# Kernel optimization log

Hardware: AMD Instinct MI355X
Metric: run time of the kernel (lower is better)

## Reference

```python
import jax, jax.numpy as jnp
import numpy as np
import math

B, T, C, H = 2, 2048, 1024, 16
HD = C // H  # head dim = 64

def setup_inputs() -> dict:
    key = jax.random.key(0)
    ks = jax.random.split(key, 12)
    s = 0.02
    return {
        "x": jax.random.normal(ks[0], (B, T, C), dtype=jnp.float32),
        "ln1_g": jnp.ones((C,), jnp.float32),
        "ln1_b": jnp.zeros((C,), jnp.float32),
        "W_attn": jax.random.normal(ks[1], (C, 3 * C), jnp.float32) * s,
        "b_attn": jnp.zeros((3 * C,), jnp.float32),
        "W_ap": jax.random.normal(ks[2], (C, C), jnp.float32) * s,
        "b_ap": jnp.zeros((C,), jnp.float32),
        "ln2_g": jnp.ones((C,), jnp.float32),
        "ln2_b": jnp.zeros((C,), jnp.float32),
        "W_fc": jax.random.normal(ks[3], (C, 4 * C), jnp.float32) * s,
        "b_fc": jnp.zeros((4 * C,), jnp.float32),
        "W_mp": jax.random.normal(ks[4], (4 * C, C), jnp.float32) * s,
        "b_mp": jnp.zeros((C,), jnp.float32),
    }

def layernorm(x, g, b, eps=1e-5):
    mu = jnp.mean(x, axis=-1, keepdims=True)
    var = jnp.mean(jnp.square(x - mu), axis=-1, keepdims=True)
    return (x - mu) * jax.lax.rsqrt(var + eps) * g + b

def gelu_tanh(x):
    # GELU(approximate='tanh')
    c = math.sqrt(2.0 / math.pi)
    return 0.5 * x * (1.0 + jnp.tanh(c * (x + 0.044715 * x * x * x)))

def attention(x, W_attn, b_attn, W_ap, b_ap):
    b, t, c = x.shape
    qkv = x @ W_attn + b_attn                      # [B,T,3C]
    q, k, v = jnp.split(qkv, 3, axis=-1)
    q = q.reshape(b, t, H, HD).transpose(0, 2, 1, 3)  # [B,H,T,hd]
    k = k.reshape(b, t, H, HD).transpose(0, 2, 1, 3)
    v = v.reshape(b, t, H, HD).transpose(0, 2, 1, 3)
    attn = jnp.einsum('bhqd,bhkd->bhqk', q, k) * (1.0 / math.sqrt(HD))
    mask = jnp.tril(jnp.ones((t, t), dtype=bool))
    attn = jnp.where(mask, attn, jnp.float32(-jnp.inf))
    attn = jax.nn.softmax(attn, axis=-1)
    y = jnp.einsum('bhqk,bhkd->bhqd', attn, v)
    y = y.transpose(0, 2, 1, 3).reshape(b, t, c)
    return y @ W_ap + b_ap

def reference(x, ln1_g, ln1_b, W_attn, b_attn, W_ap, b_ap,
              ln2_g, ln2_b, W_fc, b_fc, W_mp, b_mp):
    x = x + attention(layernorm(x, ln1_g, ln1_b), W_attn, b_attn, W_ap, b_ap)
    h = layernorm(x, ln2_g, ln2_b)
    h = gelu_tanh(h @ W_fc + b_fc) @ W_mp + b_mp
    return x + h
```

## Files before the change

kernel.cpp:

```cpp
#include <hip/hip_runtime.h>
#include <stdint.h>

#define TT_ 2048
#define CC_ 1024

typedef unsigned short u16;
typedef __bf16 bf16x8 __attribute__((ext_vector_type(8)));
typedef __bf16 bf16x4 __attribute__((ext_vector_type(4)));
typedef float f32x4 __attribute__((ext_vector_type(4)));
typedef unsigned short u16x8 __attribute__((ext_vector_type(8)));

__device__ __forceinline__ u16 f2bf(float f) {
  unsigned u = __float_as_uint(f);
  u += 0x7fff + ((u >> 16) & 1);
  return (u16)(u >> 16);
}
__device__ __forceinline__ float bf2f(u16 v) {
  return __uint_as_float(((unsigned)v) << 16);
}

__device__ __forceinline__ float gelu_f(float t) {
  float u = 1.5957691216057308f * (t + 0.044715f * t * t * t);
  return t / (1.f + __expf(-u));
}

__device__ __forceinline__ void async_cp16(const u16* g, u16* l) {
  __builtin_amdgcn_global_load_lds(
      (const __attribute__((address_space(1))) void*)(uintptr_t)g,
      (__attribute__((address_space(3))) void*)(uint32_t)(uintptr_t)l,
      16, 0, 0);
}

__device__ __forceinline__ void blockbar() {
  asm volatile("" ::: "memory");
  __builtin_amdgcn_s_barrier();
  asm volatile("" ::: "memory");
}

__global__ __launch_bounds__(256) void kconv_t(const float* __restrict__ W,
                                               u16* __restrict__ WT, int K, int N) {
  __shared__ float t[32][33];
  int n0 = blockIdx.x * 32, k0 = blockIdx.y * 32;
  int tx = threadIdx.x & 31, ty = threadIdx.x >> 5;
#pragma unroll
  for (int r = 0; r < 4; ++r)
    t[ty + 8 * r][tx] = W[(size_t)(k0 + ty + 8 * r) * N + n0 + tx];
  __syncthreads();
#pragma unroll
  for (int r = 0; r < 4; ++r)
    WT[(size_t)(n0 + ty + 8 * r) * K + k0 + tx] = f2bf(t[tx][ty + 8 * r]);
}

__global__ __launch_bounds__(256) void kln(const float* __restrict__ x,
                                           const float* __restrict__ g,
                                           const float* __restrict__ b,
                                           u16* __restrict__ out) {
  int row = blockIdx.x, tid = threadIdx.x;
  const float4* xr = (const float4*)(x + (size_t)row * CC_);
  float4 v = xr[tid];
  float s = v.x + v.y + v.z + v.w;
  float s2 = v.x * v.x + v.y * v.y + v.z * v.z + v.w * v.w;
#pragma unroll
  for (int off = 32; off; off >>= 1) { s += __shfl_down(s, off); s2 += __shfl_down(s2, off); }
  __shared__ float rs[4], rq[4];
  int w = tid >> 6;
  if ((tid & 63) == 0) { rs[w] = s; rq[w] = s2; }
  __syncthreads();
  s = rs[0] + rs[1] + rs[2] + rs[3];
  s2 = rq[0] + rq[1] + rq[2] + rq[3];
  float mean = s * (1.f / CC_);
  float var = s2 * (1.f / CC_) - mean * mean;
  float rstd = rsqrtf(var + 1e-5f);
  float4 gv = ((const float4*)g)[tid];
  float4 bv = ((const float4*)b)[tid];
  u16* orow = out + (size_t)row * CC_ + tid * 4;
  orow[0] = f2bf((v.x - mean) * rstd * gv.x + bv.x);
  orow[1] = f2bf((v.y - mean) * rstd * gv.y + bv.y);
  orow[2] = f2bf((v.z - mean) * rstd * gv.z + bv.z);
  orow[3] = f2bf((v.w - mean) * rstd * gv.w + bv.w);
}

template <int EPI, int NSPLIT>
__global__ __launch_bounds__(256) void kgemm(const u16* __restrict__ A,
                                             const u16* __restrict__ BTm,
                                             const float* __restrict__ bias,
                                             const float* __restrict__ resid,
                                             void* __restrict__ out,
                                             float* __restrict__ part,
                                             int M, int N, int Ktot) {
  __shared__ __align__(16) u16 As[2][128 * 32];
  __shared__ __align__(16) u16 Bs[2][128 * 32];
  const int tid = threadIdx.x, lane = tid & 63, w = tid >> 6;
  const int llo = lane & 15, lhi = lane >> 4;
  const int row0 = blockIdx.y * 128, col0 = blockIdx.x * 128;
  const int wr = w >> 1, wc = w & 1;
  const int crow = lane >> 2;
  const int ck = (lane & 3) * 8;
  const int Kc = Ktot / NSPLIT;
  const int klo = (NSPLIT > 1) ? blockIdx.z * Kc : 0;

  f32x4 acc[4][4] = {};

  auto stage = [&](int bufi, int kof) {
#pragma unroll
    for (int c = w; c < 8; c += 4) {
      int r = c * 16 + crow;
      async_cp16(A + (size_t)(row0 + r) * Ktot + klo + kof + ck, &As[bufi][c * 512]);
      async_cp16(BTm + (size_t)(col0 + r) * Ktot + klo + kof + ck, &Bs[bufi][c * 512]);
    }
  };

  const int nt = Kc / 32;
  stage(0, 0);
  asm volatile("s_waitcnt vmcnt(0)" ::: "memory");
  blockbar();
  int cur = 0;

  for (int t = 0; t < nt; ++t) {
    if (t + 1 < nt) stage(cur ^ 1, (t + 1) * 32);
    bf16x8 af[4], bfr[4];
#pragma unroll
    for (int m = 0; m < 4; ++m)
      af[m] = *(const bf16x8*)&As[cur][(wr * 64 + m * 16 + llo) * 32 + lhi * 8];
#pragma unroll
    for (int n = 0; n < 4; ++n)
      bfr[n] = *(const bf16x8*)&Bs[cur][(wc * 64 + n * 16 + llo) * 32 + lhi * 8];
#pragma unroll
    for (int m = 0; m < 4; ++m)
#pragma unroll
      for (int n = 0; n < 4; ++n)
        acc[m][n] = __builtin_amdgcn_mfma_f32_16x16x32_bf16(af[m], bfr[n], acc[m][n], 0, 0, 0);
    if (t + 1 < nt) {
      asm volatile("s_waitcnt vmcnt(0)" ::: "memory");
      blockbar();
    }
    cur ^= 1;
  }

  const int c_row = row0 + wr * 64 + lhi * 4;
  const int c_col = col0 + wc * 64 + llo;
  const bool fin = (NSPLIT == 1) || (blockIdx.z == 0);
#pragma unroll
  for (int n = 0; n < 4; ++n) {
    int col = c_col + n * 16;
    float bb = bias[col];
#pragma unroll
    for (int m = 0; m < 4; ++m) {
      f32x4 a = acc[m][n];
#pragma unroll
      for (int i = 0; i < 4; ++i) {
        size_t idx = (size_t)(c_row + m * 16 + i) * N + col;
        if (!fin) {
          part[idx] = a[i];
        } else {
          float val = a[i] + bb;
          if constexpr (EPI == 1) {
            ((float*)out)[idx] = val + resid[idx];
          } else if constexpr (EPI == 2) {
            ((u16*)out)[idx] = f2bf(gelu_f(val));
          } else {
            ((u16*)out)[idx] = f2bf(val);
          }
        }
      }
    }
  }
}

template <int EPI, int NSPLIT>
__global__ __launch_bounds__(512, 2) void kgemm2(const u16* __restrict__ A,
                                                 const u16* __restrict__ BTm,
                                                 const float* __restrict__ bias,
                                                 const float* __restrict__ resid,
                                                 void* __restrict__ out,
                                                 u16* __restrict__ part,
                                                 int M, int N, int Ktot) {
  __shared__ __align__(16) u16 LB[4][2][8192];
  const int tid = threadIdx.x, lane = tid & 63, w = tid >> 6;
  const int llo = lane & 15, lhi = lane >> 4;
  const int wr = w >> 2, wc = w & 3;
  const int row0 = blockIdx.y * 256, col0 = blockIdx.x * 256;
  const int Kc = Ktot / NSPLIT;
  const int klo = (NSPLIT > 1) ? blockIdx.z * Kc : 0;
  const int nt = Kc / 32;

  const int wsA = w & 3;
  const int hbB = (wc >> 1);
  const int wsB = (w & 1) + ((w >> 2) << 1);

  const u16 *gA[2], *gB[2];
  int ldsA[2], ldsB[2];
#pragma unroll
  for (int l = 0; l < 2; ++l) {
    int c = l * 256 + wsA * 64 + lane;
    int rowl = c >> 2;
    int kc = ((c & 3) ^ ((c >> 3) & 3)) * 8;
    gA[l] = A + (size_t)(row0 + wr * 128 + rowl) * Ktot + klo + kc;
    ldsA[l] = wr * 4096 + (l * 256 + wsA * 64) * 8;
    int c2 = l * 256 + wsB * 64 + lane;
    int row2 = c2 >> 2;
    int kc2 = ((c2 & 3) ^ ((c2 >> 3) & 3)) * 8;
    gB[l] = BTm + (size_t)(col0 + hbB * 128 + row2) * Ktot + klo + kc2;
    ldsB[l] = hbB * 4096 + (l * 256 + wsB * 64) * 8;
  }

  auto stage = [&](int t) {
    int slot = t & 3;
#pragma unroll
    for (int l = 0; l < 2; ++l) {
      async_cp16(gA[l] + (size_t)t * 32, &LB[slot][0][ldsA[l]]);
      async_cp16(gB[l] + (size_t)t * 32, &LB[slot][1][ldsB[l]]);
    }
  };

  f32x4 acc[8][4] = {};
  for (int t = 0; t < 3 && t < nt; ++t) stage(t);
  const int swz = (llo >> 1) & 3;
  const int aoffb = wr * 4096 + llo * 32 + (lhi ^ swz) * 8;
  const int boffb = hbB * 4096 + ((wc & 1) * 64 + llo) * 32 + (lhi ^ swz) * 8;

  for (int t = 0; t < nt; ++t) {
    const int slot = t & 3;
    const int rem = nt - 1 - t;
    if (rem >= 2)      asm volatile("s_waitcnt vmcnt(8)" ::: "memory");
    else if (rem == 1) asm volatile("s_waitcnt vmcnt(4)" ::: "memory");
    else               asm volatile("s_waitcnt vmcnt(0)" ::: "memory");
    asm volatile("s_waitcnt lgkmcnt(0)" ::: "memory");
    blockbar();
    if (t + 3 < nt) stage(t + 3);

    bf16x8 af[8], bfv[4];
#pragma unroll
    for (int n = 0; n < 4; ++n)
      bfv[n] = *(const bf16x8*)&LB[slot][1][boffb + n * 512];
#pragma unroll
    for (int m = 0; m < 8; ++m)
      af[m] = *(const bf16x8*)&LB[slot][0][aoffb + m * 512];
    __builtin_amdgcn_s_setprio(1);
#pragma unroll
    for (int m = 0; m < 8; ++m)
#pragma unroll
      for (int n = 0; n < 4; ++n)
        acc[m][n] = __builtin_amdgcn_mfma_f32_16x16x32_bf16(af[m], bfv[n], acc[m][n], 0, 0, 0);
    __builtin_amdgcn_s_setprio(0);
  }

  const int c_row0 = row0 + wr * 128 + lhi * 4;
  const int c_col0 = col0 + wc * 64 + llo;
  const bool fin = (NSPLIT == 1) || (blockIdx.z == 0);
  u16* pb = part + (NSPLIT > 1 ? ((size_t)(blockIdx.z - 1)) * M * N : 0);
#pragma unroll
  for (int n = 0; n < 4; ++n) {
    int col = c_col0 + n * 16;
    float bb = bias[col];
#pragma unroll
    for (int m = 0; m < 8; ++m) {
      f32x4 a = acc[m][n];
#pragma unroll
      for (int i = 0; i < 4; ++i) {
        size_t idx = (size_t)(c_row0 + m * 16 + i) * N + col;
        if (!fin) {
          pb[idx] = f2bf(a[i]);
        } else {
          float val = a[i] + bb;
          if constexpr (EPI == 1) {
            ((float*)out)[idx] = val + resid[idx];
          } else if constexpr (EPI == 2) {
            ((u16*)out)[idx] = f2bf(gelu_f(val));
          } else {
            ((u16*)out)[idx] = f2bf(val);
          }
        }
      }
    }
  }
}

__global__ __launch_bounds__(256) void kadd3(float* __restrict__ out,
                                             const u16* __restrict__ p, size_t MN) {
  size_t i0 = ((size_t)blockIdx.x * 256 + threadIdx.x) * 8;
  float4 o0 = *(float4*)(out + i0);
  float4 o1 = *(float4*)(out + i0 + 4);
#pragma unroll
  for (int s = 0; s < 3; ++s) {
    u16x8 v = *(const u16x8*)(p + s * MN + i0);
    o0.x += bf2f(v[0]); o0.y += bf2f(v[1]); o0.z += bf2f(v[2]); o0.w += bf2f(v[3]);
    o1.x += bf2f(v[4]); o1.y += bf2f(v[5]); o1.z += bf2f(v[6]); o1.w += bf2f(v[7]);
  }
  *(float4*)(out + i0) = o0;
  *(float4*)(out + i0 + 4) = o1;
}

__global__ __launch_bounds__(256) void kvtrans(const u16* __restrict__ qkv,
                                               u16* __restrict__ VT) {
  int tt = blockIdx.x;
  int bh = blockIdx.y;
  int b = bh >> 4, h = bh & 15;
  __shared__ u16 t[64][72];
  int r = threadIdx.x >> 3, c0 = (threadIdx.x & 7) * 8;
  const u16* src = qkv + (size_t)(b * TT_ + tt * 64) * 3072 + 2048 + h * 64;
#pragma unroll
  for (int it = 0; it < 2; ++it) {
    int rr = r + it * 32;
    *(u16x8*)&t[rr][c0] = *(const u16x8*)(src + (size_t)rr * 3072 + c0);
  }
  __syncthreads();
  u16* dst = VT + ((size_t)bh * 64) * TT_ + tt * 64;
#pragma unroll
  for (int it = 0; it < 2; ++it) {
    int d = r + it * 32;
    u16x8 v;
#pragma unroll
    for (int e = 0; e < 8; ++e) v[e] = t[c0 + e][d];
    *(u16x8*)(dst + (size_t)d * TT_ + c0) = v;
  }
}

__global__ __launch_bounds__(256, 4) void kattn(const u16* __restrict__ qkv,
                                                const u16* __restrict__ VT,
                                                u16* __restrict__ y) {
  const int h = blockIdx.x, b = blockIdx.y, z = blockIdx.z;
  const int tid = threadIdx.x, lane = tid & 63, w = tid >> 6;
  const int llo = lane & 15, lhi = lane >> 4;

  __shared__ __align__(16) u16 Qs[64 * 64];
  __shared__ __align__(16) u16 Ks[2][64 * 64];
  __shared__ __align__(16) u16 Vs[2][64 * 64];
  __shared__ __align__(16) u16 Ps[64 * 72];

  const size_t tok0 = (size_t)b * TT_;
  const u16* qb = qkv + tok0 * 3072 + h * 64;
  const u16* kb = qb + 1024;

  const u16 *kg[2], *vg[2];
#pragma unroll
  for (int it = 0; it < 2; ++it) {
    int p_ = w * 16 + it * 8 + (lane >> 3);
    int krow = ((p_ & 15) << 2) | (p_ >> 4);
    int scol = ((lane & 7) * 8) ^ ((p_ & 7) << 3);
    kg[it] = kb + (size_t)krow * 3072 + scol;
    vg[it] = VT + ((size_t)(b * 16 + h) * 64 + p_) * TT_ + scol;
  }

  auto stageKV = [&](int bufi, int j) {
    async_cp16(kg[0] + (size_t)j * (64 * 3072), &Ks[bufi][(w * 16 + 0) * 64]);
    async_cp16(kg[1] + (size_t)j * (64 * 3072), &Ks[bufi][(w * 16 + 8) * 64]);
    async_cp16(vg[0] + (size_t)j * 64, &Vs[bufi][(w * 16 + 0) * 64]);
    async_cp16(vg[1] + (size_t)j * 64, &Vs[bufi][(w * 16 + 8) * 64]);
  };

  const float alpha = 0.18033688011112042f;
  const int r8 = tid >> 3, ce = (tid & 7) * 8;

#pragma unroll 1
  for (int ph = 0; ph < 2; ++ph) {
    const int qt = ph ? (31 - z) : z;
    const int q0 = qt * 64;

#pragma unroll
    for (int it = 0; it < 2; ++it) {
      int tk = it * 32 + r8;
      u16x8 v = *(const u16x8*)(qb + (size_t)(q0 + tk) * 3072 + ce);
#pragma unroll
      for (int e = 0; e < 8; ++e) v[e] = f2bf(bf2f(v[e]) * alpha);
      *(u16x8*)&Qs[tk * 64 + (ce ^ ((tk & 7) << 3))] = v;
    }
    asm volatile("s_waitcnt lgkmcnt(0)" ::: "memory");
    stageKV(0, 0);
    blockbar();

    bf16x8 aq[2];
#pragma unroll
    for (int kk = 0; kk < 2; ++kk)
      aq[kk] = *(const bf16x8*)&Qs[(w * 16 + llo) * 64 +
                                   ((kk * 32 + lhi * 8) ^ ((llo & 7) << 3))];

    float m_i[4], l_i[4];
    f32x4 o[4] = {};
#pragma unroll
    for (int i = 0; i < 4; ++i) { m_i[i] = -1e30f; l_i[i] = 0.f; }

    int buf = 0;
    for (int j = 0; j <= qt; ++j) {
      if (j < qt) {
        stageKV(buf ^ 1, j + 1);
        asm volatile("s_waitcnt vmcnt(4)" ::: "memory");
      } else {
        asm volatile("s_waitcnt vmcnt(0)" ::: "memory");
      }
      blockbar();

      f32x4 s[4] = {};
      __builtin_amdgcn_s_setprio(1);
#pragma unroll
      for (int nb = 0; nb < 4; ++nb)
#pragma unroll
        for (int kk = 0; kk < 2; ++kk) {
          bf16x8 bk = *(const bf16x8*)&Ks[buf][(nb * 16 + llo) * 64 +
                                              ((kk * 32 + lhi * 8) ^ ((llo & 7) << 3))];
          s[nb] = __builtin_amdgcn_mfma_f32_16x16x32_bf16(aq[kk], bk, s[nb], 0, 0, 0);
        }
      __builtin_amdgcn_s_setprio(0);

      float sc[4][4];
      if (j == qt) {
#pragma unroll
        for (int nb = 0; nb < 4; ++nb)
#pragma unroll
          for (int i = 0; i < 4; ++i) {
            float v = s[nb][i];
            if (llo * 4 + nb > w * 16 + lhi * 4 + i) v = -1e30f;
            sc[nb][i] = v;
          }
      } else {
#pragma unroll
        for (int nb = 0; nb < 4; ++nb)
#pragma unroll
          for (int i = 0; i < 4; ++i) sc[nb][i] = s[nb][i];
      }

      float rm[4];
#pragma unroll
      for (int i = 0; i < 4; ++i) {
        float r = fmaxf(fmaxf(sc[0][i], sc[1][i]), fmaxf(sc[2][i], sc[3][i]));
#pragma unroll
        for (int off = 1; off < 16; off <<= 1) r = fmaxf(r, __shfl_xor(r, off));
        rm[i] = r;
      }

      bool need = (rm[0] > m_i[0] + 8.f) | (rm[1] > m_i[1] + 8.f) |
                  (rm[2] > m_i[2] + 8.f) | (rm[3] > m_i[3] + 8.f);
      if (__any(need)) {
#pragma unroll
        for (int i = 0; i < 4; ++i) {
          float mn = fmaxf(m_i[i], rm[i]);
          float corr = exp2f(m_i[i] - mn);
          l_i[i] *= corr;
#pragma unroll
          for (int db = 0; db < 4; ++db) o[db][i] *= corr;
          m_i[i] = mn;
        }
      }

#pragma unroll
      for (int i = 0; i < 4; ++i) {
        float p0 = exp2f(sc[0][i] - m_i[i]);
        float p1 = exp2f(sc[1][i] - m_i[i]);
        float p2 = exp2f(sc[2][i] - m_i[i]);
        float p3 = exp2f(sc[3][i] - m_i[i]);
        l_i[i] += (p0 + p1) + (p2 + p3);
        bf16x4 pk = {(__bf16)p0, (__bf16)p1, (__bf16)p2, (__bf16)p3};
        *(bf16x4*)&Ps[(w * 16 + lhi * 4 + i) * 72 + llo * 4] = pk;
      }

      bf16x8 pa[2];
#pragma unroll
      for (int kk = 0; kk < 2; ++kk)
        pa[kk] = *(const bf16x8*)&Ps[(w * 16 + llo) * 72 + kk * 32 + lhi * 8];
      __builtin_amdgcn_s_setprio(1);
#pragma unroll
      for (int db = 0; db < 4; ++db)
#pragma unroll
        for (int kk = 0; kk < 2; ++kk) {
          bf16x8 bv = *(const bf16x8*)&Vs[buf][(db * 16 + llo) * 64 +
                                              ((kk * 32 + lhi * 8) ^ ((llo & 7) << 3))];
          o[db] = __builtin_amdgcn_mfma_f32_16x16x32_bf16(pa[kk], bv, o[db], 0, 0, 0);
        }
      __builtin_amdgcn_s_setprio(0);
      blockbar();
      buf ^= 1;
    }

#pragma unroll
    for (int i = 0; i < 4; ++i) {
      float t = l_i[i];
#pragma unroll
      for (int off = 1; off < 16; off <<= 1) t += __shfl_xor(t, off);
      float inv = 1.f / t;
      size_t row = tok0 + q0 + w * 16 + lhi * 4 + i;
#pragma unroll
      for (int db = 0; db < 4; ++db)
        y[row * CC_ + h * 64 + db * 16 + llo] = f2bf(o[db][i] * inv);
    }
  }
}

extern "C" void kernel_launch(void* const* d_in, const int* in_sizes, int n_in,
                              void* d_out, int out_size, void* d_ws, size_t ws_size,
                              hipStream_t stream) {
  (void)in_sizes; (void)n_in; (void)out_size; (void)ws_size;
  const float* x      = (const float*)d_in[0];
  const float* ln1g   = (const float*)d_in[1];
  const float* ln1b   = (const float*)d_in[2];
  const float* W_attn = (const float*)d_in[3];
  const float* b_attn = (const float*)d_in[4];
  const float* W_ap   = (const float*)d_in[5];
  const float* b_ap   = (const float*)d_in[6];
  const float* ln2g   = (const float*)d_in[7];
  const float* ln2b   = (const float*)d_in[8];
  const float* W_fc   = (const float*)d_in[9];
  const float* b_fc   = (const float*)d_in[10];
  const float* W_mp   = (const float*)d_in[11];
  const float* b_mp   = (const float*)d_in[12];

  char* p = (char*)d_ws;
  u16* WTmp   = (u16*)p; p += (size_t)4096 * 1024 * 2;
  u16* WTattn = (u16*)p; p += (size_t)3072 * 1024 * 2;
  u16* WTap   = (u16*)p; p += (size_t)1024 * 1024 * 2;
  u16* WTfc   = (u16*)p; p += (size_t)4096 * 1024 * 2;
  u16* xn     = (u16*)p; p += (size_t)4096 * 1024 * 2;
  u16* qkvb   = (u16*)p; p += (size_t)4096 * 3072 * 2;
  u16* yb     = (u16*)p; p += (size_t)4096 * 1024 * 2;
  float* x1   = (float*)p; p += (size_t)4096 * 1024 * 4;
  u16* h2     = (u16*)p; p += (size_t)4096 * 1024 * 2;
  u16* fcb    = qkvb;
  u16* VT     = (u16*)x1;
  u16* mpp    = WTattn;

  kconv_t<<<dim3(96, 32), 256, 0, stream>>>(W_attn, WTattn, 1024, 3072);
  kconv_t<<<dim3(32, 32), 256, 0, stream>>>(W_ap, WTap, 1024, 1024);
  kconv_t<<<dim3(128, 32), 256, 0, stream>>>(W_fc, WTfc, 1024, 4096);
  kconv_t<<<dim3(32, 128), 256, 0, stream>>>(W_mp, WTmp, 4096, 1024);

  kln<<<4096, 256, 0, stream>>>(x, ln1g, ln1b, xn);
  kgemm<0, 1><<<dim3(24, 32), 256, 0, stream>>>(xn, WTattn, b_attn, nullptr, qkvb, nullptr, 4096, 3072, 1024);
  kvtrans<<<dim3(32, 32), 256, 0, stream>>>(qkvb, VT);
  kattn<<<dim3(16, 2, 16), 256, 0, stream>>>(qkvb, VT, yb);
  kgemm<1, 1><<<dim3(8, 32), 256, 0, stream>>>(yb, WTap, b_ap, x, x1, nullptr, 4096, 1024, 1024);
  kln<<<4096, 256, 0, stream>>>(x1, ln2g, ln2b, h2);
  kgemm2<2, 1><<<dim3(16, 16), 512, 0, stream>>>(h2, WTfc, b_fc, nullptr, fcb, nullptr, 4096, 4096, 1024);
  kgemm2<1, 4><<<dim3(4, 16, 4), 512, 0, stream>>>(fcb, WTmp, b_mp, x1, (float*)d_out, mpp, 4096, 1024, 4096);
  kadd3<<<2048, 256, 0, stream>>>((float*)d_out, mpp, (size_t)4096 * 1024);
}
```

Measured before the change: 273.8 us.

## Replace 256-tile GEMM with 128-tile kernel and split-K the attention projection

Deletes the 256x256 four-stage pipelined kgemm2 kernel and runs the FC and MLP-projection GEMMs on the simpler 128x128 double-buffered kgemm. The attention output projection is now split-K by two, with bf16 partials reduced by a generalized add kernel. kgemm's partial buffer changes from fp32 to bf16 per-split slabs. This gives more blocks for occupancy but loses the larger tile's data reuse and deeper pipeline, and adds an extra reduction pass plus bf16 rounding of the partial sums.

```diff
diff --git a/kernel.cpp b/kernel.cpp
--- a/kernel.cpp
+++ b/kernel.cpp
@@ -86,7 +86,7 @@
                                              const float* __restrict__ bias,
                                              const float* __restrict__ resid,
                                              void* __restrict__ out,
-                                             float* __restrict__ part,
+                                             u16* __restrict__ part,
                                              int M, int N, int Ktot) {
   __shared__ __align__(16) u16 As[2][128 * 32];
   __shared__ __align__(16) u16 Bs[2][128 * 32];
@@ -140,6 +140,7 @@
   const int c_row = row0 + wr * 64 + lhi * 4;
   const int c_col = col0 + wc * 64 + llo;
   const bool fin = (NSPLIT == 1) || (blockIdx.z == 0);
+  u16* pb = part + (NSPLIT > 1 ? ((size_t)(blockIdx.z > 0 ? blockIdx.z - 1 : 0)) * M * N : 0);
 #pragma unroll
   for (int n = 0; n < 4; ++n) {
     int col = c_col + n * 16;
@@ -150,115 +151,6 @@
 #pragma unroll
       for (int i = 0; i < 4; ++i) {
         size_t idx = (size_t)(c_row + m * 16 + i) * N + col;
-        if (!fin) {
-          part[idx] = a[i];
-        } else {
-          float val = a[i] + bb;
-          if constexpr (EPI == 1) {
-            ((float*)out)[idx] = val + resid[idx];
-          } else if constexpr (EPI == 2) {
-            ((u16*)out)[idx] = f2bf(gelu_f(val));
-          } else {
-            ((u16*)out)[idx] = f2bf(val);
-          }
-        }
-      }
-    }
-  }
-}
-
-template <int EPI, int NSPLIT>
-__global__ __launch_bounds__(512, 2) void kgemm2(const u16* __restrict__ A,
-                                                 const u16* __restrict__ BTm,
-                                                 const float* __restrict__ bias,
-                                                 const float* __restrict__ resid,
-                                                 void* __restrict__ out,
-                                                 u16* __restrict__ part,
-                                                 int M, int N, int Ktot) {
-  __shared__ __align__(16) u16 LB[4][2][8192];
-  const int tid = threadIdx.x, lane = tid & 63, w = tid >> 6;
-  const int llo = lane & 15, lhi = lane >> 4;
-  const int wr = w >> 2, wc = w & 3;
-  const int row0 = blockIdx.y * 256, col0 = blockIdx.x * 256;
-  const int Kc = Ktot / NSPLIT;
-  const int klo = (NSPLIT > 1) ? blockIdx.z * Kc : 0;
-  const int nt = Kc / 32;
-
-  const int wsA = w & 3;
-  const int hbB = (wc >> 1);
-  const int wsB = (w & 1) + ((w >> 2) << 1);
-
-  const u16 *gA[2], *gB[2];
-  int ldsA[2], ldsB[2];
-#pragma unroll
-  for (int l = 0; l < 2; ++l) {
-    int c = l * 256 + wsA * 64 + lane;
-    int rowl = c >> 2;
-    int kc = ((c & 3) ^ ((c >> 3) & 3)) * 8;
-    gA[l] = A + (size_t)(row0 + wr * 128 + rowl) * Ktot + klo + kc;
-    ldsA[l] = wr * 4096 + (l * 256 + wsA * 64) * 8;
-    int c2 = l * 256 + wsB * 64 + lane;
-    int row2 = c2 >> 2;
-    int kc2 = ((c2 & 3) ^ ((c2 >> 3) & 3)) * 8;
-    gB[l] = BTm + (size_t)(col0 + hbB * 128 + row2) * Ktot + klo + kc2;
-    ldsB[l] = hbB * 4096 + (l * 256 + wsB * 64) * 8;
-  }
-
-  auto stage = [&](int t) {
-    int slot = t & 3;
-#pragma unroll
-    for (int l = 0; l < 2; ++l) {
-      async_cp16(gA[l] + (size_t)t * 32, &LB[slot][0][ldsA[l]]);
-      async_cp16(gB[l] + (size_t)t * 32, &LB[slot][1][ldsB[l]]);
-    }
-  };
-
-  f32x4 acc[8][4] = {};
-  for (int t = 0; t < 3 && t < nt; ++t) stage(t);
-  const int swz = (llo >> 1) & 3;
-  const int aoffb = wr * 4096 + llo * 32 + (lhi ^ swz) * 8;
-  const int boffb = hbB * 4096 + ((wc & 1) * 64 + llo) * 32 + (lhi ^ swz) * 8;
-
-  for (int t = 0; t < nt; ++t) {
-    const int slot = t & 3;
-    const int rem = nt - 1 - t;
-    if (rem >= 2)      asm volatile("s_waitcnt vmcnt(8)" ::: "memory");
-    else if (rem == 1) asm volatile("s_waitcnt vmcnt(4)" ::: "memory");
-    else               asm volatile("s_waitcnt vmcnt(0)" ::: "memory");
-    asm volatile("s_waitcnt lgkmcnt(0)" ::: "memory");
-    blockbar();
-    if (t + 3 < nt) stage(t + 3);
-
-    bf16x8 af[8], bfv[4];
-#pragma unroll
-    for (int n = 0; n < 4; ++n)
-      bfv[n] = *(const bf16x8*)&LB[slot][1][boffb + n * 512];
-#pragma unroll
-    for (int m = 0; m < 8; ++m)
-      af[m] = *(const bf16x8*)&LB[slot][0][aoffb + m * 512];
-    __builtin_amdgcn_s_setprio(1);
-#pragma unroll
-    for (int m = 0; m < 8; ++m)
-#pragma unroll
-      for (int n = 0; n < 4; ++n)
-        acc[m][n] = __builtin_amdgcn_mfma_f32_16x16x32_bf16(af[m], bfv[n], acc[m][n], 0, 0, 0);
-    __builtin_amdgcn_s_setprio(0);
-  }
-
-  const int c_row0 = row0 + wr * 128 + lhi * 4;
-  const int c_col0 = col0 + wc * 64 + llo;
-  const bool fin = (NSPLIT == 1) || (blockIdx.z == 0);
-  u16* pb = part + (NSPLIT > 1 ? ((size_t)(blockIdx.z - 1)) * M * N : 0);
-#pragma unroll
-  for (int n = 0; n < 4; ++n) {
-    int col = c_col0 + n * 16;
-    float bb = bias[col];
-#pragma unroll
-    for (int m = 0; m < 8; ++m) {
-      f32x4 a = acc[m][n];
-#pragma unroll
-      for (int i = 0; i < 4; ++i) {
-        size_t idx = (size_t)(c_row0 + m * 16 + i) * N + col;
         if (!fin) {
           pb[idx] = f2bf(a[i]);
         } else {
@@ -276,14 +168,15 @@
   }
 }
 
-__global__ __launch_bounds__(256) void kadd3(float* __restrict__ out,
+template <int NP>
+__global__ __launch_bounds__(256) void kaddN(float* __restrict__ out,
                                              const u16* __restrict__ p, size_t MN) {
   size_t i0 = ((size_t)blockIdx.x * 256 + threadIdx.x) * 8;
   float4 o0 = *(float4*)(out + i0);
   float4 o1 = *(float4*)(out + i0 + 4);
 #pragma unroll
-  for (int s = 0; s < 3; ++s) {
-    u16x8 v = *(const u16x8*)(p + s * MN + i0);
+  for (int s = 0; s < NP; ++s) {
+    u16x8 v = *(const u16x8*)(p + (size_t)s * MN + i0);
     o0.x += bf2f(v[0]); o0.y += bf2f(v[1]); o0.z += bf2f(v[2]); o0.w += bf2f(v[3]);
     o1.x += bf2f(v[4]); o1.y += bf2f(v[5]); o1.z += bf2f(v[6]); o1.w += bf2f(v[7]);
   }
@@ -515,6 +408,7 @@
   u16* h2     = (u16*)p; p += (size_t)4096 * 1024 * 2;
   u16* fcb    = qkvb;
   u16* VT     = (u16*)x1;
+  u16* appart = xn;
   u16* mpp    = WTattn;
 
   kconv_t<<<dim3(96, 32), 256, 0, stream>>>(W_attn, WTattn, 1024, 3072);
@@ -526,9 +420,10 @@
   kgemm<0, 1><<<dim3(24, 32), 256, 0, stream>>>(xn, WTattn, b_attn, nullptr, qkvb, nullptr, 4096, 3072, 1024);
   kvtrans<<<dim3(32, 32), 256, 0, stream>>>(qkvb, VT);
   kattn<<<dim3(16, 2, 16), 256, 0, stream>>>(qkvb, VT, yb);
-  kgemm<1, 1><<<dim3(8, 32), 256, 0, stream>>>(yb, WTap, b_ap, x, x1, nullptr, 4096, 1024, 1024);
+  kgemm<1, 2><<<dim3(8, 32, 2), 256, 0, stream>>>(yb, WTap, b_ap, x, x1, appart, 4096, 1024, 1024);
+  kaddN<1><<<2048, 256, 0, stream>>>(x1, appart, (size_t)4096 * 1024);
   kln<<<4096, 256, 0, stream>>>(x1, ln2g, ln2b, h2);
-  kgemm2<2, 1><<<dim3(16, 16), 512, 0, stream>>>(h2, WTfc, b_fc, nullptr, fcb, nullptr, 4096, 4096, 1024);
-  kgemm2<1, 4><<<dim3(4, 16, 4), 512, 0, stream>>>(fcb, WTmp, b_mp, x1, (float*)d_out, mpp, 4096, 1024, 4096);
-  kadd3<<<2048, 256, 0, stream>>>((float*)d_out, mpp, (size_t)4096 * 1024);
-}
+  kgemm<2, 1><<<dim3(32, 32), 256, 0, stream>>>(h2, WTfc, b_fc, nullptr, fcb, nullptr, 4096, 4096, 1024);
+  kgemm<1, 4><<<dim3(8, 32, 4), 256, 0, stream>>>(fcb, WTmp, b_mp, x1, (float*)d_out, mpp, 4096, 1024, 4096);
+  kaddN<3><<<2048, 256, 0, stream>>>((float*)d_out, mpp, (size_t)4096 * 1024);
+}
```

Measured after the change: 299.6 us. +9.4%, slower.
